# Kernel tuning notes

Hardware: AMD Instinct MI355X
Metric: run time of the kernel (lower is better)

The kernel has to match this reference:

```python
import jax, jax.numpy as jnp
import numpy as np

POOLED_H = 7
POOLED_W = 7
SPATIAL_SCALE = 0.0625


def setup_inputs() -> dict:
    key = jax.random.key(0)
    kf, kb, kc = jax.random.split(key, 3)
    B, C, H, W = 2, 256, 100, 100
    N = 256
    features = jax.random.normal(kf, (B, C, H, W), jnp.float32)
    batch_idx = jax.random.randint(kb, (N,), 0, B).astype(jnp.float32)
    img = H / SPATIAL_SCALE  # image-space extent (1600)
    c = jax.random.uniform(kc, (N, 4), jnp.float32, 0.0, img - 32.0)
    x1 = jnp.minimum(c[:, 0], c[:, 2])
    x2 = jnp.maximum(c[:, 0], c[:, 2]) + 16.0
    y1 = jnp.minimum(c[:, 1], c[:, 3])
    y2 = jnp.maximum(c[:, 1], c[:, 3]) + 16.0
    rois = jnp.stack([batch_idx, x1, y1, x2, y2], axis=1)
    return {"features": features, "rois": rois}


def _hat_cdf(u):
    # antiderivative of the unit hat function phi(u)=max(0,1-|u|), Phi(-inf)=0
    return jnp.where(
        u <= 0.0,
        0.5 * jnp.clip(u + 1.0, 0.0, 1.0) ** 2,
        1.0 - 0.5 * jnp.clip(1.0 - u, 0.0, 1.0) ** 2,
    )


def _bin_weights(lo, hi, size):
    # lo, hi: [N, P] bin boundaries in feature coords -> weights [N, P, size]
    # w[n,p,j] = integral over [lo,hi] of the linear-interp hat centered at j
    idx = jnp.arange(size, dtype=lo.dtype)
    return _hat_cdf(hi[..., None] - idx) - _hat_cdf(lo[..., None] - idx)


def reference(features, rois):
    # Precise RoI Pooling: exact integral of the bilinearly interpolated
    # feature map over each bin, divided by the bin area. Bilinear interp is
    # a tensor product of 1D hats, so the 2D integral separates:
    #   out[n,c,p,q] = (1/area) * sum_{h,w} F[bi,c,h,w] * wy[n,p,h] * wx[n,q,w]
    B, C, H, W = features.shape
    N = rois.shape[0]
    bi = rois[:, 0].astype(jnp.int32)
    x1 = rois[:, 1] * SPATIAL_SCALE
    y1 = rois[:, 2] * SPATIAL_SCALE
    x2 = rois[:, 3] * SPATIAL_SCALE
    y2 = rois[:, 4] * SPATIAL_SCALE
    bw = (x2 - x1) / POOLED_W
    bh = (y2 - y1) / POOLED_H
    ph = jnp.arange(POOLED_H, dtype=rois.dtype)
    pw = jnp.arange(POOLED_W, dtype=rois.dtype)
    ylo = y1[:, None] + ph * bh[:, None]
    yhi = ylo + bh[:, None]
    xlo = x1[:, None] + pw * bw[:, None]
    xhi = xlo + bw[:, None]
    wy = _bin_weights(ylo, yhi, H)  # [N, P, H]
    wx = _bin_weights(xlo, xhi, W)  # [N, Q, W]
    out = jnp.zeros((N, C, POOLED_H, POOLED_W), features.dtype)
    for b in range(B):  # small fixed loop over batch images
        wyb = wy * (bi == b).astype(wy.dtype)[:, None, None]
        out = out + jnp.einsum('chw,nph,nqw->ncpq', features[b], wyb, wx)
    area = jnp.maximum(bw * bh, 0.0)
    out = jnp.where(
        area[:, None, None, None] > 0,
        out / jnp.maximum(area, 1e-12)[:, None, None, None],
        0.0,
    )
    return out
```

## Files before the change

### kernel.cpp

```cpp
#include <hip/hip_runtime.h>
#include <hip/hip_bf16.h>

#define POOLED 7
#define PP 49
#define SCALE 0.0625f
#define RMAX 20
#define QMAX 24
#define TW 256

__device__ __forceinline__ float hat_cdf(float u) {
  if (u <= 0.0f) {
    float t = fminf(fmaxf(u + 1.0f, 0.0f), 1.0f);
    return 0.5f * t * t;
  } else {
    float t = fminf(fmaxf(1.0f - u, 0.0f), 1.0f);
    return 1.0f - 0.5f * t * t;
  }
}

__device__ __forceinline__ float bf_lo(uint32_t u) { return __uint_as_float(u << 16); }
__device__ __forceinline__ float bf_hi(uint32_t u) { return __uint_as_float(u & 0xffff0000u); }

#define FMA4(A, U, WT) do { \
  (A)[0] = fmaf(bf_lo((U).x), (WT), (A)[0]); (A)[1] = fmaf(bf_hi((U).x), (WT), (A)[1]); \
  (A)[2] = fmaf(bf_lo((U).y), (WT), (A)[2]); (A)[3] = fmaf(bf_hi((U).y), (WT), (A)[3]); \
} while (0)

__global__ __launch_bounds__(256)
void transpose_bf16_kernel(const float* __restrict__ in,
                           __hip_bfloat16* __restrict__ out, int C, int S) {
  __shared__ float tile[32][33];
  int b  = blockIdx.z;
  int s0 = blockIdx.x * 32;
  int c0 = blockIdx.y * 32;
  const float* inb = in + (size_t)b * C * S;
  __hip_bfloat16* outb = out + (size_t)b * S * C;
  int tx = threadIdx.x, ty = threadIdx.y;
#pragma unroll
  for (int j = 0; j < 4; j++) {
    int c = c0 + ty + j * 8, s = s0 + tx;
    tile[ty + j * 8][tx] = (c < C && s < S) ? inb[(size_t)c * S + s] : 0.0f;
  }
  __syncthreads();
#pragma unroll
  for (int j = 0; j < 4; j++) {
    int s = s0 + ty + j * 8, c = c0 + tx;
    if (s < S && c < C) outb[(size_t)s * C + c] = __float2bfloat16(tile[tx][ty + j * 8]);
  }
}

__global__ __launch_bounds__(TW, 4)
void prroi_kernel(const __hip_bfloat16* __restrict__ ft,
                  const float* __restrict__ rois,
                  float* __restrict__ out, int N, int C, int H, int W) {
  __shared__ float s_wx[QMAX];
  __shared__ float s_wy[RMAX];
  __shared__ float s_red[4 * 64 * 5];

  int nb = gridDim.x;
  int bid = blockIdx.x;
  if ((nb & 7) == 0) {
    int cpx = nb >> 3;
    bid = (bid & 7) * cpx + (bid >> 3);
  }
  int n = bid / PP;
  int pq = bid - n * PP;
  int p = pq / POOLED, q = pq - p * POOLED;

  int tid = threadIdx.x;
  int wave = tid >> 6, lane = tid & 63;

  float bif = rois[n * 5 + 0];
  float x1  = rois[n * 5 + 1] * SCALE;
  float y1  = rois[n * 5 + 2] * SCALE;
  float x2  = rois[n * 5 + 3] * SCALE;
  float y2  = rois[n * 5 + 4] * SCALE;
  int bi = (int)bif;
  float bw = (x2 - x1) * (1.0f / POOLED);
  float bh = (y2 - y1) * (1.0f / POOLED);
  float ylo = y1 + p * bh, yhi = ylo + bh;
  float xlo = x1 + q * bw, xhi = xlo + bw;

  int h0 = max(0, (int)floorf(ylo));
  int h1 = min(H - 1, (int)ceilf(yhi));
  int rows = h1 - h0 + 1;
  if (rows > RMAX) rows = RMAX;
  int w0 = max(0, (int)floorf(xlo));
  int w1 = min(W - 1, (int)ceilf(xhi));
  int nw = w1 - w0 + 1;
  if (nw > QMAX) nw = QMAX;

  float area = fmaxf(bw * bh, 0.0f);
  float inv_area = (area > 0.0f) ? 1.0f / fmaxf(area, 1e-12f) : 0.0f;

  for (int i = tid; i < nw; i += TW) {
    float j = (float)(w0 + i);
    s_wx[i] = (hat_cdf(xhi - j) - hat_cdf(xlo - j)) * inv_area;
  }
  for (int i = tid; i < rows; i += TW) {
    float j = (float)(h0 + i);
    s_wy[i] = hat_cdf(yhi - j) - hat_cdf(ylo - j);
  }
  __syncthreads();

  float acc[4] = {0.0f, 0.0f, 0.0f, 0.0f};

  const int C4 = C >> 2;
  const uint2* lp = (const uint2*)ft + ((size_t)bi * H * W) * C4 + lane;

  for (int ih = wave; ih < rows; ih += 8) {
    int iA = ih, iB = ih + 4;
    float wyA = s_wy[iA];
    float wyB = (iB < rows) ? s_wy[iB] : 0.0f;
    if (wyA == 0.0f && wyB == 0.0f) continue;
    if (wyA == 0.0f) { wyA = wyB; wyB = 0.0f; iA = iB; }
    bool bOK = (wyB != 0.0f);

    const uint2* rpA = lp + (size_t)((h0 + iA) * W + w0) * C4;
    const uint2* rpB = bOK ? lp + (size_t)((h0 + iB) * W + w0) * C4 : rpA;

    int iw = 0;
    if (bOK) {
      for (; iw + 3 < nw; iw += 4) {
        float wx0 = s_wx[iw], wx1 = s_wx[iw + 1], wx2 = s_wx[iw + 2], wx3 = s_wx[iw + 3];
        uint2 uA0 = rpA[(size_t)iw * C4];
        uint2 uA1 = rpA[(size_t)(iw + 1) * C4];
        uint2 uA2 = rpA[(size_t)(iw + 2) * C4];
        uint2 uA3 = rpA[(size_t)(iw + 3) * C4];
        uint2 uB0 = rpB[(size_t)iw * C4];
        uint2 uB1 = rpB[(size_t)(iw + 1) * C4];
        uint2 uB2 = rpB[(size_t)(iw + 2) * C4];
        uint2 uB3 = rpB[(size_t)(iw + 3) * C4];
        FMA4(acc, uA0, wyA * wx0); FMA4(acc, uA1, wyA * wx1);
        FMA4(acc, uA2, wyA * wx2); FMA4(acc, uA3, wyA * wx3);
        FMA4(acc, uB0, wyB * wx0); FMA4(acc, uB1, wyB * wx1);
        FMA4(acc, uB2, wyB * wx2); FMA4(acc, uB3, wyB * wx3);
      }
      for (; iw < nw; iw++) {
        float wx0 = s_wx[iw];
        uint2 uA = rpA[(size_t)iw * C4];
        uint2 uB = rpB[(size_t)iw * C4];
        FMA4(acc, uA, wyA * wx0);
        FMA4(acc, uB, wyB * wx0);
      }
    } else {
      for (; iw + 3 < nw; iw += 4) {
        float wx0 = s_wx[iw], wx1 = s_wx[iw + 1], wx2 = s_wx[iw + 2], wx3 = s_wx[iw + 3];
        uint2 uA0 = rpA[(size_t)iw * C4];
        uint2 uA1 = rpA[(size_t)(iw + 1) * C4];
        uint2 uA2 = rpA[(size_t)(iw + 2) * C4];
        uint2 uA3 = rpA[(size_t)(iw + 3) * C4];
        FMA4(acc, uA0, wyA * wx0); FMA4(acc, uA1, wyA * wx1);
        FMA4(acc, uA2, wyA * wx2); FMA4(acc, uA3, wyA * wx3);
      }
      for (; iw < nw; iw++) {
        float wx0 = s_wx[iw];
        uint2 uA = rpA[(size_t)iw * C4];
        FMA4(acc, uA, wyA * wx0);
      }
    }
  }

  float* slot = s_red + (size_t)(wave * 64 + lane) * 5;
#pragma unroll
  for (int k = 0; k < 4; k++) slot[k] = acc[k];
  __syncthreads();

  int c = tid;
  int base = (c >> 2) * 5 + (c & 3);
  float v = s_red[base] + s_red[base + 64 * 5] +
            s_red[base + 2 * 64 * 5] + s_red[base + 3 * 64 * 5];
  out[((size_t)n * C + c) * PP + pq] = v;
}

__global__ void prroi_fallback(const float* __restrict__ feat,
                               const float* __restrict__ rois,
                               float* __restrict__ out, int N, int C, int H, int W) {
  int idx = blockIdx.x * blockDim.x + threadIdx.x;
  if (idx >= N * C * PP) return;
  int n = idx / (C * PP), r = idx % (C * PP);
  int c = r / PP, pq = r % PP;
  int p = pq / POOLED, q = pq % POOLED;
  float x1 = rois[n * 5 + 1] * SCALE, y1 = rois[n * 5 + 2] * SCALE;
  float x2 = rois[n * 5 + 3] * SCALE, y2 = rois[n * 5 + 4] * SCALE;
  int bi = (int)rois[n * 5 + 0];
  float bw = (x2 - x1) / POOLED, bh = (y2 - y1) / POOLED;
  float xlo = x1 + q * bw, xhi = xlo + bw;
  float ylo = y1 + p * bh, yhi = ylo + bh;
  float area = fmaxf(bw * bh, 0.0f);
  float inv_area = (area > 0.0f) ? 1.0f / fmaxf(area, 1e-12f) : 0.0f;
  const float* f = feat + ((size_t)bi * C + c) * H * W;
  float acc = 0.0f;
  int h0 = max(0, (int)floorf(ylo)), h1 = min(H - 1, (int)ceilf(yhi));
  int w0 = max(0, (int)floorf(xlo)), w1 = min(W - 1, (int)ceilf(xhi));
  for (int h = h0; h <= h1; h++) {
    float wy = hat_cdf(yhi - h) - hat_cdf(ylo - h);
    for (int w = w0; w <= w1; w++) {
      float wx = hat_cdf(xhi - w) - hat_cdf(xlo - w);
      acc += f[h * W + w] * wy * wx;
    }
  }
  out[idx] = acc * inv_area;
}

extern "C" void kernel_launch(void* const* d_in, const int* in_sizes, int n_in,
                              void* d_out, int out_size, void* d_ws, size_t ws_size,
                              hipStream_t stream) {
  const float* feat = (const float*)d_in[0];
  const float* rois = (const float*)d_in[1];
  float* out = (float*)d_out;

  const int B = 2, H = 100, W = 100, S = H * W;
  int N = in_sizes[1] / 5;
  int C = out_size / (N * PP);

  size_t need = (size_t)B * S * C * sizeof(__hip_bfloat16);
  if (C == 256 && ws_size >= need) {
    __hip_bfloat16* ft = (__hip_bfloat16*)d_ws;
    dim3 tb(32, 8);
    dim3 tg((S + 31) / 32, (C + 31) / 32, B);
    transpose_bf16_kernel<<<tg, tb, 0, stream>>>(feat, ft, C, S);
    prroi_kernel<<<N * PP, TW, 0, stream>>>(ft, rois, out, N, C, H, W);
  } else {
    int total = N * C * PP;
    prroi_fallback<<<(total + 255) / 256, 256, 0, stream>>>(feat, rois, out, N, C, H, W);
  }
}
```

Measured before the change: 52.73 us.

## Use 16-byte bf16 loads with half-wave column split in PrRoI kernel

```diff
diff --git a/kernel.cpp b/kernel.cpp
--- a/kernel.cpp
+++ b/kernel.cpp
@@ -21,9 +21,11 @@
 __device__ __forceinline__ float bf_lo(uint32_t u) { return __uint_as_float(u << 16); }
 __device__ __forceinline__ float bf_hi(uint32_t u) { return __uint_as_float(u & 0xffff0000u); }
 
-#define FMA4(A, U, WT) do { \
+#define FMA8(A, U, WT) do { \
   (A)[0] = fmaf(bf_lo((U).x), (WT), (A)[0]); (A)[1] = fmaf(bf_hi((U).x), (WT), (A)[1]); \
   (A)[2] = fmaf(bf_lo((U).y), (WT), (A)[2]); (A)[3] = fmaf(bf_hi((U).y), (WT), (A)[3]); \
+  (A)[4] = fmaf(bf_lo((U).z), (WT), (A)[4]); (A)[5] = fmaf(bf_hi((U).z), (WT), (A)[5]); \
+  (A)[6] = fmaf(bf_lo((U).w), (WT), (A)[6]); (A)[7] = fmaf(bf_hi((U).w), (WT), (A)[7]); \
 } while (0)
 
 __global__ __launch_bounds__(256)
@@ -55,7 +57,7 @@
                   float* __restrict__ out, int N, int C, int H, int W) {
   __shared__ float s_wx[QMAX];
   __shared__ float s_wy[RMAX];
-  __shared__ float s_red[4 * 64 * 5];
+  __shared__ float s_red[4 * 32 * 9];
 
   int nb = gridDim.x;
   int bid = blockIdx.x;
@@ -69,6 +71,8 @@
 
   int tid = threadIdx.x;
   int wave = tid >> 6, lane = tid & 63;
+  int l5 = lane >> 5;
+  int l31 = lane & 31;
 
   float bif = rois[n * 5 + 0];
   float x1  = rois[n * 5 + 1] * SCALE;
@@ -88,14 +92,18 @@
   int w0 = max(0, (int)floorf(xlo));
   int w1 = min(W - 1, (int)ceilf(xhi));
   int nw = w1 - w0 + 1;
-  if (nw > QMAX) nw = QMAX;
+  if (nw > QMAX - 1) nw = QMAX - 1;
 
   float area = fmaxf(bw * bh, 0.0f);
   float inv_area = (area > 0.0f) ? 1.0f / fmaxf(area, 1e-12f) : 0.0f;
 
-  for (int i = tid; i < nw; i += TW) {
-    float j = (float)(w0 + i);
-    s_wx[i] = (hat_cdf(xhi - j) - hat_cdf(xlo - j)) * inv_area;
+  for (int i = tid; i < QMAX; i += TW) {
+    float v = 0.0f;
+    if (i < nw) {
+      float j = (float)(w0 + i);
+      v = (hat_cdf(xhi - j) - hat_cdf(xlo - j)) * inv_area;
+    }
+    s_wx[i] = v;
   }
   for (int i = tid; i < rows; i += TW) {
     float j = (float)(h0 + i);
@@ -103,10 +111,14 @@
   }
   __syncthreads();
 
-  float acc[4] = {0.0f, 0.0f, 0.0f, 0.0f};
-
-  const int C4 = C >> 2;
-  const uint2* lp = (const uint2*)ft + ((size_t)bi * H * W) * C4 + lane;
+  float acc[8];
+#pragma unroll
+  for (int k = 0; k < 8; k++) acc[k] = 0.0f;
+
+  const int C8 = C >> 3;
+  const uint4* lp = (const uint4*)ft + ((size_t)bi * H * W) * C8 + l31;
+  const int ns = (nw + 1) >> 1;
+  const int cmax = nw - 1;
 
   for (int ih = wave; ih < rows; ih += 8) {
     int iA = ih, iB = ih + 4;
@@ -116,60 +128,66 @@
     if (wyA == 0.0f) { wyA = wyB; wyB = 0.0f; iA = iB; }
     bool bOK = (wyB != 0.0f);
 
-    const uint2* rpA = lp + (size_t)((h0 + iA) * W + w0) * C4;
-    const uint2* rpB = bOK ? lp + (size_t)((h0 + iB) * W + w0) * C4 : rpA;
-
-    int iw = 0;
+    const uint4* rpA = lp + (size_t)((h0 + iA) * W + w0) * C8;
+    const uint4* rpB = bOK ? lp + (size_t)((h0 + iA + 4) * W + w0) * C8 : rpA;
+
+    int s = 0;
     if (bOK) {
-      for (; iw + 3 < nw; iw += 4) {
-        float wx0 = s_wx[iw], wx1 = s_wx[iw + 1], wx2 = s_wx[iw + 2], wx3 = s_wx[iw + 3];
-        uint2 uA0 = rpA[(size_t)iw * C4];
-        uint2 uA1 = rpA[(size_t)(iw + 1) * C4];
-        uint2 uA2 = rpA[(size_t)(iw + 2) * C4];
-        uint2 uA3 = rpA[(size_t)(iw + 3) * C4];
-        uint2 uB0 = rpB[(size_t)iw * C4];
-        uint2 uB1 = rpB[(size_t)(iw + 1) * C4];
-        uint2 uB2 = rpB[(size_t)(iw + 2) * C4];
-        uint2 uB3 = rpB[(size_t)(iw + 3) * C4];
-        FMA4(acc, uA0, wyA * wx0); FMA4(acc, uA1, wyA * wx1);
-        FMA4(acc, uA2, wyA * wx2); FMA4(acc, uA3, wyA * wx3);
-        FMA4(acc, uB0, wyB * wx0); FMA4(acc, uB1, wyB * wx1);
-        FMA4(acc, uB2, wyB * wx2); FMA4(acc, uB3, wyB * wx3);
-      }
-      for (; iw < nw; iw++) {
-        float wx0 = s_wx[iw];
-        uint2 uA = rpA[(size_t)iw * C4];
-        uint2 uB = rpB[(size_t)iw * C4];
-        FMA4(acc, uA, wyA * wx0);
-        FMA4(acc, uB, wyB * wx0);
+      for (; s + 1 < ns; s += 2) {
+        int i0 = (s << 1) + l5;
+        int i1 = i0 + 2;
+        int c0i = min(i0, cmax), c1i = min(i1, cmax);
+        uint4 uA0 = rpA[(size_t)c0i * C8];
+        uint4 uA1 = rpA[(size_t)c1i * C8];
+        uint4 uB0 = rpB[(size_t)c0i * C8];
+        uint4 uB1 = rpB[(size_t)c1i * C8];
+        float wf0 = s_wx[i0], wf1 = s_wx[i1];
+        FMA8(acc, uA0, wyA * wf0); FMA8(acc, uA1, wyA * wf1);
+        FMA8(acc, uB0, wyB * wf0); FMA8(acc, uB1, wyB * wf1);
+      }
+      if (s < ns) {
+        int i0 = (s << 1) + l5;
+        int c0i = min(i0, cmax);
+        uint4 uA = rpA[(size_t)c0i * C8];
+        uint4 uB = rpB[(size_t)c0i * C8];
+        float wf0 = s_wx[i0];
+        FMA8(acc, uA, wyA * wf0);
+        FMA8(acc, uB, wyB * wf0);
       }
     } else {
-      for (; iw + 3 < nw; iw += 4) {
-        float wx0 = s_wx[iw], wx1 = s_wx[iw + 1], wx2 = s_wx[iw + 2], wx3 = s_wx[iw + 3];
-        uint2 uA0 = rpA[(size_t)iw * C4];
-        uint2 uA1 = rpA[(size_t)(iw + 1) * C4];
-        uint2 uA2 = rpA[(size_t)(iw + 2) * C4];
-        uint2 uA3 = rpA[(size_t)(iw + 3) * C4];
-        FMA4(acc, uA0, wyA * wx0); FMA4(acc, uA1, wyA * wx1);
-        FMA4(acc, uA2, wyA * wx2); FMA4(acc, uA3, wyA * wx3);
-      }
-      for (; iw < nw; iw++) {
-        float wx0 = s_wx[iw];
-        uint2 uA = rpA[(size_t)iw * C4];
-        FMA4(acc, uA, wyA * wx0);
+      for (; s + 1 < ns; s += 2) {
+        int i0 = (s << 1) + l5;
+        int i1 = i0 + 2;
+        int c0i = min(i0, cmax), c1i = min(i1, cmax);
+        uint4 uA0 = rpA[(size_t)c0i * C8];
+        uint4 uA1 = rpA[(size_t)c1i * C8];
+        float wf0 = s_wx[i0], wf1 = s_wx[i1];
+        FMA8(acc, uA0, wyA * wf0); FMA8(acc, uA1, wyA * wf1);
+      }
+      if (s < ns) {
+        int i0 = (s << 1) + l5;
+        int c0i = min(i0, cmax);
+        uint4 uA = rpA[(size_t)c0i * C8];
+        float wf0 = s_wx[i0];
+        FMA8(acc, uA, wyA * wf0);
       }
     }
   }
 
-  float* slot = s_red + (size_t)(wave * 64 + lane) * 5;
-#pragma unroll
-  for (int k = 0; k < 4; k++) slot[k] = acc[k];
+#pragma unroll
+  for (int k = 0; k < 8; k++) acc[k] += __shfl_xor(acc[k], 32, 64);
+
+  if (l5 == 0) {
+    float* slot = s_red + (size_t)(wave * 32 + l31) * 9;
+#pragma unroll
+    for (int k = 0; k < 8; k++) slot[k] = acc[k];
+  }
   __syncthreads();
 
   int c = tid;
-  int base = (c >> 2) * 5 + (c & 3);
-  float v = s_red[base] + s_red[base + 64 * 5] +
-            s_red[base + 2 * 64 * 5] + s_red[base + 3 * 64 * 5];
+  int base = (c >> 3) * 9 + (c & 7);
+  float v = s_red[base] + s_red[base + 32 * 9] +
+            s_red[base + 2 * 32 * 9] + s_red[base + 3 * 32 * 9];
   out[((size_t)n * C + c) * PP + pq] = v;
 }
 
```

Result: faster. 47.59 us (-9.7%).
